# Optimization experiments

Measured on AMD Instinct MI355X. Metric: run time of the kernel, lower is better.

## Reference

```python
import jax, jax.numpy as jnp
import numpy as np

N_NODES = 100000


def gcn_conv(x, W, b, src, dst, n_nodes):
    # Linear transform first (PyG GCNConv applies weight before propagation)
    h = x @ W  # [N, out]
    # gcn_norm with self-loops: deg[i] = 1 + #incoming edges at i
    ones = jnp.ones(src.shape[0], dtype=h.dtype)
    deg = jax.ops.segment_sum(ones, dst, num_segments=n_nodes) + 1.0
    dinv = jax.lax.rsqrt(deg)  # deg^{-1/2}, deg >= 1 so safe
    norm = dinv[src] * dinv[dst]  # [E]
    # aggregate normalized messages at destination nodes
    agg = jax.ops.segment_sum(h[src] * norm[:, None], dst, num_segments=n_nodes)
    # self-loop contribution: norm_ii = dinv[i]^2
    agg = agg + h * (dinv * dinv)[:, None]
    return agg + b


def setup_inputs() -> dict:
    key = jax.random.key(0)
    k1, k2, k3, k4, k5, k6 = jax.random.split(key, 6)
    num_features, hidden, num_classes = 512, 128, 64
    x = jax.random.normal(k1, (N_NODES, num_features), dtype=jnp.float32)
    edge_index = jax.random.randint(k2, (2, 1600000), 0, N_NODES, dtype=jnp.int64)
    # Glorot-style params (scaled normals)
    W1 = jax.random.normal(k3, (num_features, hidden), dtype=jnp.float32) / np.sqrt(num_features)
    b1 = jnp.zeros((hidden,), dtype=jnp.float32)
    W2 = jax.random.normal(k4, (hidden, num_classes), dtype=jnp.float32) / np.sqrt(hidden)
    b2 = jnp.zeros((num_classes,), dtype=jnp.float32)
    return {"x": x, "edge_index": edge_index, "W1": W1, "b1": b1, "W2": W2, "b2": b2}


def reference(x, edge_index, W1, b1, W2, b2):
    src, dst = edge_index[0], edge_index[1]
    h = jax.nn.relu(gcn_conv(x, W1, b1, src, dst, N_NODES))
    out = gcn_conv(h, W2, b2, src, dst, N_NODES)
    return jax.nn.log_softmax(out, axis=1)
```

## Files before the change

### kernel.cpp

```cpp
#include <hip/hip_runtime.h>
#include <cmath>

#define N_NODES 100000
#define N_EDGES 1600000
#define F_IN 512
#define F_HID 128
#define F_OUT 64

#define BK_SHIFT 10
#define NBUK ((N_NODES + 1023) >> 10)
#define SCAP 24576
#define LSLOT 64
#define NBLK_A 512
#define FILL_SPLIT 8
#define NPS (1024 / FILL_SPLIT)
#define OV_CAP 4096

typedef __attribute__((ext_vector_type(8))) short short8;
typedef __attribute__((ext_vector_type(4))) float float4v;
typedef __attribute__((ext_vector_type(2))) float f2v;

#define GLOAD_LDS16(g, l)                                                      \
    __builtin_amdgcn_global_load_lds(                                          \
        (const __attribute__((address_space(1))) void*)(g),                    \
        (__attribute__((address_space(3))) void*)(l), 16, 0, 0)

__device__ __forceinline__ unsigned short f2bf(float f) {
    unsigned u = __builtin_bit_cast(unsigned, f);
    u += 0x7FFFu + ((u >> 16) & 1u);
    return (unsigned short)(u >> 16);
}
__device__ __forceinline__ float lo_bf(unsigned u) {
    return __builtin_bit_cast(float, u << 16);
}
__device__ __forceinline__ float hi_bf(unsigned u) {
    return __builtin_bit_cast(float, u & 0xFFFF0000u);
}
__device__ __forceinline__ f2v bfpair(unsigned u) {
    return f2v{__builtin_bit_cast(float, u << 16),
               __builtin_bit_cast(float, u & 0xFFFF0000u)};
}
__device__ __forceinline__ short8 cvt8(float4 lo, float4 hi) {
    return short8{(short)f2bf(lo.x), (short)f2bf(lo.y), (short)f2bf(lo.z), (short)f2bf(lo.w),
                  (short)f2bf(hi.x), (short)f2bf(hi.y), (short)f2bf(hi.z), (short)f2bf(hi.w)};
}
__device__ __forceinline__ unsigned pack_bf2(float a, float b) {
    return (unsigned)f2bf(a) | ((unsigned)f2bf(b) << 16);
}

template <int N>
__device__ __forceinline__ void waitvm() {
    if constexpr (N == 0) asm volatile("s_waitcnt vmcnt(0)" ::: "memory");
    else if constexpr (N == 3) asm volatile("s_waitcnt vmcnt(3)" ::: "memory");
    else if constexpr (N == 6) asm volatile("s_waitcnt vmcnt(6)" ::: "memory");
    else static_assert(N == 0 || N == 3 || N == 6, "add literal");
}
#define LGKM0() asm volatile("s_waitcnt lgkmcnt(0)" ::: "memory")
#define BAR() __builtin_amdgcn_s_barrier()
#define SCHED0() __builtin_amdgcn_sched_barrier(0)

__global__ __launch_bounds__(256) void partition_kernel(
    const int* __restrict__ src, const int* __restrict__ dst,
    unsigned* __restrict__ staging, int* __restrict__ gcur,
    unsigned long long* __restrict__ ovbuf, int* __restrict__ ovcnt) {
    __shared__ unsigned buf[NBUK][LSLOT];
    __shared__ int cnt[NBUK];
    int tid = threadIdx.x;
    for (int b = tid; b < NBUK; b += 256) cnt[b] = 0;
    __syncthreads();
    constexpr int PER = (((N_EDGES + NBLK_A - 1) / NBLK_A) + 3) & ~3;
    int e0 = blockIdx.x * PER;
    int e1 = min(e0 + PER, N_EDGES);

    auto body = [&](int d, int s) {
        int b = d >> BK_SHIFT;
        unsigned rec = (unsigned)s | ((unsigned)(d & 1023) << 17);
        int slot = atomicAdd(&cnt[b], 1);
        if (slot < LSLOT) {
            buf[b][slot] = rec;
        } else {
            int op = atomicAdd(ovcnt, 1);
            if (op < OV_CAP)
                ovbuf[op] = ((unsigned long long)(unsigned)d << 32) | (unsigned)s;
        }
    };
    auto drain = [&](void) {
        for (int b = tid; b < NBUK; b += 256) {
            int c = min(cnt[b], LSLOT);
            int full = c & ~15;
            if (full > 0) {
                int pos = atomicAdd(&gcur[b], full);
                if (pos + full <= SCAP) {
                    unsigned* dp = &staging[(size_t)b * SCAP + pos];
                    for (int i = 0; i < full; ++i) dp[i] = buf[b][i];
                }
                for (int i = 0; i < c - full; ++i) buf[b][i] = buf[b][full + i];
            }
            cnt[b] = c - full;
        }
    };

    int base = e0;
    for (; base + 1024 <= e1; base += 1024) {
        int e = base + tid * 4;
        int4 dv = *(const int4*)(dst + e);
        int4 sv = *(const int4*)(src + e);
        body(dv.x, sv.x);
        body(dv.y, sv.y);
        body(dv.z, sv.z);
        body(dv.w, sv.w);
        __syncthreads();
        drain();
        __syncthreads();
    }
    for (int e = base + tid; e < e1; e += 256) body(dst[e], src[e]);
    __syncthreads();
    drain();
    __syncthreads();
    for (int b = tid; b < NBUK; b += 256) {
        int c = cnt[b];
        if (c > 0) {
            int pos = atomicAdd(&gcur[b], c);
            if (pos + c <= SCAP)
                for (int i = 0; i < c; ++i) staging[(size_t)b * SCAP + pos + i] = buf[b][i];
        }
    }
}

__global__ __launch_bounds__(128) void bucket_scan_kernel(
    const int* __restrict__ gcur, const unsigned long long* __restrict__ ovbuf,
    const int* __restrict__ ovcnt, int* __restrict__ bucket_base,
    int* __restrict__ row_ptr) {
    __shared__ int ovc[128];
    __shared__ int sc[128];
    int tid = threadIdx.x;
    ovc[tid] = 0;
    int tot = (tid < NBUK) ? min(gcur[tid], SCAP) : 0;
    __syncthreads();
    int oc = *ovcnt;
    if (oc > OV_CAP) oc = OV_CAP;
    for (int k = tid; k < oc; k += 128)
        atomicAdd(&ovc[(int)(ovbuf[k] >> 32) >> BK_SHIFT], 1);
    __syncthreads();
    int v = tot + ovc[tid];
    sc[tid] = v;
    __syncthreads();
    for (int d = 1; d < 128; d <<= 1) {
        int u = (tid >= d) ? sc[tid - d] : 0;
        __syncthreads();
        sc[tid] += u;
        __syncthreads();
    }
    if (tid < NBUK) bucket_base[tid] = sc[tid] - v;
    if (tid == NBUK - 1) {
        bucket_base[NBUK] = sc[tid];
        row_ptr[N_NODES] = sc[tid];
    }
}

__global__ __launch_bounds__(256) void deg_hist_row_kernel(
    const unsigned* __restrict__ staging, const int* __restrict__ gcur,
    const unsigned long long* __restrict__ ovbuf, const int* __restrict__ ovcnt,
    const int* __restrict__ bucket_base, int* __restrict__ row_ptr,
    float* __restrict__ dinv) {
    int b = blockIdx.x;
    __shared__ int hist[1024];
    __shared__ int psum[256];
    int tid = threadIdx.x;
    for (int i = tid; i < 1024; i += 256) hist[i] = 0;
    __syncthreads();
    int n = gcur[b];
    if (n > SCAP) n = SCAP;
    const unsigned* sp = &staging[(size_t)b * SCAP];
    int i = tid * 4;
    for (; i + 4 <= n; i += 1024) {
        uint4 r = *(const uint4*)(sp + i);
        atomicAdd(&hist[r.x >> 17], 1);
        atomicAdd(&hist[r.y >> 17], 1);
        atomicAdd(&hist[r.z >> 17], 1);
        atomicAdd(&hist[r.w >> 17], 1);
    }
    int tail0 = n & ~3;
    if (tid < (n - tail0)) atomicAdd(&hist[sp[tail0 + tid] >> 17], 1);
    int oc = *ovcnt;
    if (oc > OV_CAP) oc = OV_CAP;
    for (int k = tid; k < oc; k += 256) {
        int d = (int)(ovbuf[k] >> 32);
        if ((d >> BK_SHIFT) == b) atomicAdd(&hist[d & 1023], 1);
    }
    __syncthreads();
    int i4 = tid * 4;
    int s0 = hist[i4], s1 = hist[i4 + 1], s2 = hist[i4 + 2], s3 = hist[i4 + 3];
    int ms = s0 + s1 + s2 + s3;
    psum[tid] = ms;
    __syncthreads();
    for (int d = 1; d < 256; d <<= 1) {
        int u = (tid >= d) ? psum[tid - d] : 0;
        __syncthreads();
        psum[tid] += u;
        __syncthreads();
    }
    int ex = psum[tid] - ms + bucket_base[b];
    int nd = (b << BK_SHIFT) + i4;
    if (nd < N_NODES) {
        row_ptr[nd]     = ex;
        row_ptr[nd + 1] = ex + s0;
        row_ptr[nd + 2] = ex + s0 + s1;
        row_ptr[nd + 3] = ex + s0 + s1 + s2;
        dinv[nd]     = rsqrtf((float)(s0 + 1));
        dinv[nd + 1] = rsqrtf((float)(s1 + 1));
        dinv[nd + 2] = rsqrtf((float)(s2 + 1));
        dinv[nd + 3] = rsqrtf((float)(s3 + 1));
    }
}

__global__ __launch_bounds__(256) void fill_kernel(
    const unsigned* __restrict__ staging, const int* __restrict__ gcur,
    const int* __restrict__ row_ptr, int* __restrict__ csr_src,
    const unsigned long long* __restrict__ ovbuf, const int* __restrict__ ovcnt) {
    int b = blockIdx.x / FILL_SPLIT;
    int slice = blockIdx.x - b * FILL_SPLIT;
    int dl0 = slice * NPS;
    int node0 = (b << BK_SHIFT) + dl0;
    __shared__ int lcur[NPS];
    int tid = threadIdx.x;
    if (tid < NPS) {
        int nd = node0 + tid;
        lcur[tid] = (nd < N_NODES) ? row_ptr[nd] : 0;
    }
    __syncthreads();

    int n = gcur[b];
    if (n > SCAP) n = SCAP;
    const unsigned* sp = &staging[(size_t)b * SCAP];

    auto process = [&](unsigned rec) {
        int dl = (int)(rec >> 17) - dl0;
        if ((unsigned)dl < (unsigned)NPS) {
            int pos = atomicAdd(&lcur[dl], 1);
            csr_src[pos] = (int)(rec & 0x1FFFFu);
        }
    };

    int i = tid * 4;
    for (; i + 4 <= n; i += 1024) {
        uint4 r = *(const uint4*)(sp + i);
        process(r.x);
        process(r.y);
        process(r.z);
        process(r.w);
    }
    int tail0 = n & ~3;
    if (tid < (n - tail0)) process(sp[tail0 + tid]);

    int oc = *ovcnt;
    if (oc > OV_CAP) oc = OV_CAP;
    for (int k = tid; k < oc; k += 256) {
        unsigned long long r = ovbuf[k];
        int d = (int)(r >> 32);
        int dl = d - node0;
        if ((d >> BK_SHIFT) == b && (unsigned)dl < (unsigned)NPS) {
            int pos = atomicAdd(&lcur[dl], 1);
            csr_src[pos] = (int)(r & 0xffffffffu);
        }
    }
}


__global__ void transpose_w_kernel(const float* __restrict__ W1, const float* __restrict__ W2,
                                   unsigned short* __restrict__ Wt1,
                                   unsigned short* __restrict__ Wt2) {
    int g = blockIdx.x * 256 + threadIdx.x;
    if (g < F_HID * F_IN) {
        int n = g >> 9, k = g & 511;
        Wt1[g] = f2bf(W1[k * F_HID + n]);
    } else {
        int h = g - F_HID * F_IN;
        if (h < F_OUT * F_HID) {
            int n = h >> 7, k = h & 127;
            Wt2[h] = f2bf(W2[k * F_OUT + n]);
        }
    }
}


template <int BN, int K, bool A_BF16>
__global__ __launch_bounds__(256, 3) void gemm_lds_kernel(
    const void* __restrict__ Araw, const unsigned short* __restrict__ Wt,
    const float* __restrict__ dinv, unsigned short* __restrict__ out, int N) {
    constexpr int NCT = BN / 16;
    constexpr int AE = A_BF16 ? 2 : 4;
    constexpr int SLOTS_A = (32 * AE) / 16;
    constexpr int MA = SLOTS_A - 1;
    constexpr int ABYTES = 128 * 32 * AE;
    constexpr int BBYTES = BN * 32 * 2;
    constexpr int NT = K / 32;
    constexpr int SL = (128 * SLOTS_A + BN * 4) / 256;

    __shared__ __align__(128) char Abuf[2][ABYTES];
    __shared__ __align__(128) char Bbuf[2][BBYTES];

    const char* Ab = (const char*)Araw;
    const char* Bb = (const char*)Wt;
    int tid = threadIdx.x;
    int lane = tid & 63;
    int wv = tid >> 6;
    int row0 = blockIdx.x * 128;
    int l15 = lane & 15;
    int q = lane >> 4;

    float4v acc[2][NCT] = {};

    auto stage = [&](int buf, int k0) {
        constexpr int CA = 128 * SLOTS_A;
#pragma unroll
        for (int i = 0; i < CA / 256; ++i) {
            int c = i * 256 + tid;
            int cw = i * 256 + (tid & ~63);
            int row = c / SLOTS_A;
            int s = c & MA;
            int g = s ^ (row & MA);
            int rg = row0 + row;
            if (rg >= N) rg = N - 1;
            GLOAD_LDS16(Ab + ((size_t)rg * K + k0) * AE + g * 16,
                        &Abuf[buf][cw * 16]);
        }
        constexpr int CB = BN * 4;
#pragma unroll
        for (int i = 0; i < CB / 256; ++i) {
            int c = i * 256 + tid;
            int cw = i * 256 + (tid & ~63);
            int col = c >> 2;
            int s = c & 3;
            int g = s ^ (col & 3);
            GLOAD_LDS16(Bb + ((size_t)col * K + k0) * 2 + g * 16,
                        &Bbuf[buf][cw * 16]);
        }
    };

    auto compute = [&](int buf) {
        const char* Ac = Abuf[buf];
        const char* Bc = Bbuf[buf];
        int lr0 = wv * 32 + l15;
        int lr1 = lr0 + 16;
        short8 a0, a1;
        if constexpr (A_BF16) {
            int s0 = q ^ (lr0 & 3);
            int s1 = q ^ (lr1 & 3);
            a0 = *(const short8*)(Ac + lr0 * 64 + s0 * 16);
            a1 = *(const short8*)(Ac + lr1 * 64 + s1 * 16);
        } else {
            int r7a = lr0 & 7, r7b = lr1 & 7;
            float4 f0 = *(const float4*)(Ac + lr0 * 128 + ((2 * q) ^ r7a) * 16);
            float4 f1 = *(const float4*)(Ac + lr0 * 128 + ((2 * q + 1) ^ r7a) * 16);
            float4 f2 = *(const float4*)(Ac + lr1 * 128 + ((2 * q) ^ r7b) * 16);
            float4 f3 = *(const float4*)(Ac + lr1 * 128 + ((2 * q + 1) ^ r7b) * 16);
            a0 = cvt8(f0, f1);
            a1 = cvt8(f2, f3);
        }
#pragma unroll
        for (int ct = 0; ct < NCT; ++ct) {
            int col = ct * 16 + l15;
            int sb = q ^ (col & 3);
            short8 b = *(const short8*)(Bc + col * 64 + sb * 16);
            acc[0][ct] = __builtin_amdgcn_mfma_f32_16x16x32_bf16(a0, b, acc[0][ct], 0, 0, 0);
            acc[1][ct] = __builtin_amdgcn_mfma_f32_16x16x32_bf16(a1, b, acc[1][ct], 0, 0, 0);
        }
    };

    stage(0, 0);
    stage(1, 32);
#pragma unroll 1
    for (int t = 0; t < NT - 2; ++t) {
        waitvm<SL>();
        BAR();
        SCHED0();
        compute(t & 1);
        LGKM0();
        BAR();
        SCHED0();
        stage(t & 1, (t + 2) * 32);
    }
    waitvm<SL>();
    BAR();
    SCHED0();
    compute((NT - 2) & 1);
    waitvm<0>();
    BAR();
    SCHED0();
    compute((NT - 1) & 1);

#pragma unroll
    for (int rt = 0; rt < 2; ++rt) {
#pragma unroll
        for (int reg = 0; reg < 4; ++reg) {
            int row = row0 + wv * 32 + rt * 16 + q * 4 + reg;
            if (row < N) {
                float sc = dinv[row];
#pragma unroll
                for (int ct = 0; ct < NCT; ++ct) {
                    out[(size_t)row * BN + ct * 16 + l15] = f2bf(acc[rt][ct][reg] * sc);
                }
            }
        }
    }
}


__global__ __launch_bounds__(256) void agg1_kernel(
    const uint4* __restrict__ g1v, const int* __restrict__ row_ptr,
    const int* __restrict__ csr_src, const float* __restrict__ dinv,
    const float4* __restrict__ b1v, uint4* __restrict__ h1v) {
    int tid = threadIdx.x;
    int wv = tid >> 6;
    int lane = tid & 63;
    int qt = lane >> 4;
    int ql = lane & 15;
    int node = blockIdx.x * 16 + wv * 4 + qt;
    uint4 u = g1v[(size_t)node * 16 + ql];
    f2v A0 = bfpair(u.x), A1 = bfpair(u.y), A2 = bfpair(u.z), A3 = bfpair(u.w);
    int e = row_ptr[node], end = row_ptr[node + 1];
#define GA1(j) g1v[(size_t)(j) * 16 + ql]
#define ACCV(v)                                                                \
    do { A0 += bfpair((v).x); A1 += bfpair((v).y);                             \
         A2 += bfpair((v).z); A3 += bfpair((v).w); } while (0)
    if (e + 8 <= end) {
        int j0 = csr_src[e], j1 = csr_src[e + 1], j2 = csr_src[e + 2], j3 = csr_src[e + 3];
        int j4 = csr_src[e + 4], j5 = csr_src[e + 5], j6 = csr_src[e + 6], j7 = csr_src[e + 7];
        uint4 v0 = GA1(j0), v1 = GA1(j1), v2 = GA1(j2), v3 = GA1(j3);
        uint4 v4 = GA1(j4), v5 = GA1(j5), v6 = GA1(j6), v7 = GA1(j7);
        e += 8;
        for (; e + 8 <= end; e += 8) {
            int k0 = csr_src[e], k1 = csr_src[e + 1], k2 = csr_src[e + 2], k3 = csr_src[e + 3];
            int k4 = csr_src[e + 4], k5 = csr_src[e + 5], k6 = csr_src[e + 6], k7 = csr_src[e + 7];
            ACCV(v0); ACCV(v1); ACCV(v2); ACCV(v3);
            ACCV(v4); ACCV(v5); ACCV(v6); ACCV(v7);
            v0 = GA1(k0); v1 = GA1(k1); v2 = GA1(k2); v3 = GA1(k3);
            v4 = GA1(k4); v5 = GA1(k5); v6 = GA1(k6); v7 = GA1(k7);
        }
        ACCV(v0); ACCV(v1); ACCV(v2); ACCV(v3);
        ACCV(v4); ACCV(v5); ACCV(v6); ACCV(v7);
    }
    for (; e < end; ++e) {
        uint4 v = GA1(csr_src[e]);
        ACCV(v);
    }
#undef ACCV
#undef GA1
    float d = dinv[node];
    float4 ba = b1v[2 * ql], bb = b1v[2 * ql + 1];
    float r0 = fmaxf(d * A0.x + ba.x, 0.0f), r1 = fmaxf(d * A0.y + ba.y, 0.0f);
    float r2 = fmaxf(d * A1.x + ba.z, 0.0f), r3 = fmaxf(d * A1.y + ba.w, 0.0f);
    float r4 = fmaxf(d * A2.x + bb.x, 0.0f), r5 = fmaxf(d * A2.y + bb.y, 0.0f);
    float r6 = fmaxf(d * A3.x + bb.z, 0.0f), r7 = fmaxf(d * A3.y + bb.w, 0.0f);
    h1v[(size_t)node * 16 + ql] =
        uint4{pack_bf2(r0, r1), pack_bf2(r2, r3), pack_bf2(r4, r5), pack_bf2(r6, r7)};
}

__global__ __launch_bounds__(256) void agg2_lsm_kernel(
    const uint2* __restrict__ g2v, const int* __restrict__ row_ptr,
    const int* __restrict__ csr_src, const float* __restrict__ dinv,
    const float4* __restrict__ b2v, float4* __restrict__ outv) {
    int tid = threadIdx.x;
    int wv = tid >> 6;
    int lane = tid & 63;
    int qt = lane >> 4;
    int ql = lane & 15;
    int node = blockIdx.x * 16 + wv * 4 + qt;
    uint2 u = g2v[(size_t)node * 16 + ql];
    f2v A0 = bfpair(u.x), A1 = bfpair(u.y);
    int e = row_ptr[node], end = row_ptr[node + 1];
#define GA2(j) g2v[(size_t)(j) * 16 + ql]
#define ACCV(v) do { A0 += bfpair((v).x); A1 += bfpair((v).y); } while (0)
    if (e + 8 <= end) {
        int j0 = csr_src[e], j1 = csr_src[e + 1], j2 = csr_src[e + 2], j3 = csr_src[e + 3];
        int j4 = csr_src[e + 4], j5 = csr_src[e + 5], j6 = csr_src[e + 6], j7 = csr_src[e + 7];
        uint2 v0 = GA2(j0), v1 = GA2(j1), v2 = GA2(j2), v3 = GA2(j3);
        uint2 v4 = GA2(j4), v5 = GA2(j5), v6 = GA2(j6), v7 = GA2(j7);
        e += 8;
        for (; e + 8 <= end; e += 8) {
            int k0 = csr_src[e], k1 = csr_src[e + 1], k2 = csr_src[e + 2], k3 = csr_src[e + 3];
            int k4 = csr_src[e + 4], k5 = csr_src[e + 5], k6 = csr_src[e + 6], k7 = csr_src[e + 7];
            ACCV(v0); ACCV(v1); ACCV(v2); ACCV(v3);
            ACCV(v4); ACCV(v5); ACCV(v6); ACCV(v7);
            v0 = GA2(k0); v1 = GA2(k1); v2 = GA2(k2); v3 = GA2(k3);
            v4 = GA2(k4); v5 = GA2(k5); v6 = GA2(k6); v7 = GA2(k7);
        }
        ACCV(v0); ACCV(v1); ACCV(v2); ACCV(v3);
        ACCV(v4); ACCV(v5); ACCV(v6); ACCV(v7);
    }
    for (; e < end; ++e) {
        uint2 v = GA2(csr_src[e]);
        ACCV(v);
    }
#undef ACCV
#undef GA2
    float d = dinv[node];
    float4 b = b2v[ql];
    float v0 = d * A0.x + b.x;
    float v1 = d * A0.y + b.y;
    float v2 = d * A1.x + b.z;
    float v3 = d * A1.y + b.w;
    float m = fmaxf(fmaxf(v0, v1), fmaxf(v2, v3));
#pragma unroll
    for (int o = 8; o > 0; o >>= 1) m = fmaxf(m, __shfl_xor(m, o, 64));
    float s = __expf(v0 - m) + __expf(v1 - m) + __expf(v2 - m) + __expf(v3 - m);
#pragma unroll
    for (int o = 8; o > 0; o >>= 1) s += __shfl_xor(s, o, 64);
    float ls = m + __logf(s);
    outv[(size_t)node * 16 + ql] = float4{v0 - ls, v1 - ls, v2 - ls, v3 - ls};
}


extern "C" void kernel_launch(void* const* d_in, const int* in_sizes, int n_in,
                              void* d_out, int out_size, void* d_ws, size_t ws_size,
                              hipStream_t stream) {
    const float* x  = (const float*)d_in[0];
    const int* eidx = (const int*)d_in[1];
    const float* W1 = (const float*)d_in[2];
    const float* b1 = (const float*)d_in[3];
    const float* W2 = (const float*)d_in[4];
    const float* b2 = (const float*)d_in[5];
    float* out = (float*)d_out;
    const int* src = eidx;
    const int* dst = eidx + N_EDGES;

    char* base = (char*)d_ws;
    size_t off = 0;
    auto alloc = [&](size_t bytes) -> void* {
        void* p = base + off;
        off += (bytes + 255) & ~(size_t)255;
        return p;
    };
    int* zbase    = (int*)alloc((size_t)(NBUK + 64) * 4);
    int* gcur     = zbase;
    int* ovcnt    = zbase + NBUK;
    int* bucket_base = (int*)alloc((size_t)(NBUK + 1) * 4);
    int* row_ptr  = (int*)alloc((size_t)(N_NODES + 1) * 4);
    float* dinv   = (float*)alloc((size_t)N_NODES * 4);
    unsigned* staging = (unsigned*)alloc((size_t)NBUK * SCAP * 4);
    unsigned long long* ovbuf = (unsigned long long*)alloc((size_t)OV_CAP * 8);
    int* csr_src  = (int*)alloc((size_t)N_EDGES * 4);
    unsigned short* Wt1 = (unsigned short*)alloc((size_t)F_HID * F_IN * 2);
    unsigned short* Wt2 = (unsigned short*)alloc((size_t)F_OUT * F_HID * 2);
    unsigned short* g1  = (unsigned short*)alloc((size_t)N_NODES * F_HID * 2);
    unsigned short* h1  = (unsigned short*)alloc((size_t)N_NODES * F_HID * 2);
    unsigned short* g2  = g1;

    hipMemsetAsync(zbase, 0, (size_t)(NBUK + 64) * 4, stream);
    partition_kernel<<<NBLK_A, 256, 0, stream>>>(src, dst, staging, gcur, ovbuf, ovcnt);
    bucket_scan_kernel<<<1, 128, 0, stream>>>(gcur, ovbuf, ovcnt, bucket_base, row_ptr);
    deg_hist_row_kernel<<<NBUK, 256, 0, stream>>>(staging, gcur, ovbuf, ovcnt,
                                                  bucket_base, row_ptr, dinv);
    fill_kernel<<<NBUK * FILL_SPLIT, 256, 0, stream>>>(staging, gcur, row_ptr, csr_src,
                                                       ovbuf, ovcnt);
    transpose_w_kernel<<<(F_HID * F_IN + F_OUT * F_HID + 255) / 256, 256, 0, stream>>>(
        W1, W2, Wt1, Wt2);

    int gblocks = (N_NODES + 127) / 128;
    gemm_lds_kernel<F_HID, F_IN, false><<<gblocks, 256, 0, stream>>>(
        (const void*)x, Wt1, dinv, g1, N_NODES);
    agg1_kernel<<<N_NODES / 16, 256, 0, stream>>>(
        (const uint4*)g1, row_ptr, csr_src, dinv, (const float4*)b1, (uint4*)h1);

    gemm_lds_kernel<F_OUT, F_HID, true><<<gblocks, 256, 0, stream>>>(
        (const void*)h1, Wt2, dinv, g2, N_NODES);
    agg2_lsm_kernel<<<N_NODES / 16, 256, 0, stream>>>(
        (const uint2*)g2, row_ptr, csr_src, dinv, (const float4*)b2, (float4*)out);
}
```

Baseline: 504.0 us.

## Replace incremental bucket drain with per-block fixed segments and count table

The partition kernel no longer drains its LDS buckets to global staging every 1024 edges with global atomics. Instead each block keeps up to 64 records per bucket in LDS and writes its whole buffer once to a private fixed segment, plus a per-bucket count table. The scan, histogram and fill kernels read the per-block segments using these counts. This removes repeated barriers, serial drain loops and global atomics, in exchange for sparse strided reads of a larger staging area and more reliance on the overflow buffer.

Measured after the change: 493.9 us. 2.0% less time.

```diff
diff --git a/kernel.cpp b/kernel.cpp
--- a/kernel.cpp
+++ b/kernel.cpp
@@ -9,9 +9,9 @@
 
 #define BK_SHIFT 10
 #define NBUK ((N_NODES + 1023) >> 10)
-#define SCAP 24576
-#define LSLOT 64
 #define NBLK_A 512
+#define PCAP 64
+#define SEGW (NBUK * PCAP)
 #define FILL_SPLIT 8
 #define NPS (1024 / FILL_SPLIT)
 #define OV_CAP 4096
@@ -61,9 +61,9 @@
 
 __global__ __launch_bounds__(256) void partition_kernel(
     const int* __restrict__ src, const int* __restrict__ dst,
-    unsigned* __restrict__ staging, int* __restrict__ gcur,
+    unsigned* __restrict__ staging, int* __restrict__ cnt_t,
     unsigned long long* __restrict__ ovbuf, int* __restrict__ ovcnt) {
-    __shared__ unsigned buf[NBUK][LSLOT];
+    __shared__ __align__(16) unsigned buf[NBUK][PCAP];
     __shared__ int cnt[NBUK];
     int tid = threadIdx.x;
     for (int b = tid; b < NBUK; b += 256) cnt[b] = 0;
@@ -76,27 +76,12 @@
         int b = d >> BK_SHIFT;
         unsigned rec = (unsigned)s | ((unsigned)(d & 1023) << 17);
         int slot = atomicAdd(&cnt[b], 1);
-        if (slot < LSLOT) {
+        if (slot < PCAP) {
             buf[b][slot] = rec;
         } else {
             int op = atomicAdd(ovcnt, 1);
             if (op < OV_CAP)
                 ovbuf[op] = ((unsigned long long)(unsigned)d << 32) | (unsigned)s;
-        }
-    };
-    auto drain = [&](void) {
-        for (int b = tid; b < NBUK; b += 256) {
-            int c = min(cnt[b], LSLOT);
-            int full = c & ~15;
-            if (full > 0) {
-                int pos = atomicAdd(&gcur[b], full);
-                if (pos + full <= SCAP) {
-                    unsigned* dp = &staging[(size_t)b * SCAP + pos];
-                    for (int i = 0; i < full; ++i) dp[i] = buf[b][i];
-                }
-                for (int i = 0; i < c - full; ++i) buf[b][i] = buf[b][full + i];
-            }
-            cnt[b] = c - full;
         }
     };
 
@@ -109,33 +94,32 @@
         body(dv.y, sv.y);
         body(dv.z, sv.z);
         body(dv.w, sv.w);
-        __syncthreads();
-        drain();
-        __syncthreads();
     }
     for (int e = base + tid; e < e1; e += 256) body(dst[e], src[e]);
     __syncthreads();
-    drain();
-    __syncthreads();
-    for (int b = tid; b < NBUK; b += 256) {
-        int c = cnt[b];
-        if (c > 0) {
-            int pos = atomicAdd(&gcur[b], c);
-            if (pos + c <= SCAP)
-                for (int i = 0; i < c; ++i) staging[(size_t)b * SCAP + pos + i] = buf[b][i];
-        }
-    }
+    const uint4* lb = (const uint4*)buf;
+    uint4* dp = (uint4*)(staging + (size_t)blockIdx.x * SEGW);
+    for (int i = tid; i < SEGW / 4; i += 256) dp[i] = lb[i];
+    for (int b = tid; b < NBUK; b += 256)
+        cnt_t[(size_t)b * NBLK_A + blockIdx.x] = min(cnt[b], PCAP);
 }
 
 __global__ __launch_bounds__(128) void bucket_scan_kernel(
-    const int* __restrict__ gcur, const unsigned long long* __restrict__ ovbuf,
+    const int* __restrict__ cnt_t, const unsigned long long* __restrict__ ovbuf,
     const int* __restrict__ ovcnt, int* __restrict__ bucket_base,
     int* __restrict__ row_ptr) {
     __shared__ int ovc[128];
     __shared__ int sc[128];
     int tid = threadIdx.x;
     ovc[tid] = 0;
-    int tot = (tid < NBUK) ? min(gcur[tid], SCAP) : 0;
+    int tot = 0;
+    if (tid < NBUK) {
+        const int4* p = (const int4*)(cnt_t + (size_t)tid * NBLK_A);
+        for (int i = 0; i < NBLK_A / 4; ++i) {
+            int4 v = p[i];
+            tot += v.x + v.y + v.z + v.w;
+        }
+    }
     __syncthreads();
     int oc = *ovcnt;
     if (oc > OV_CAP) oc = OV_CAP;
@@ -159,29 +143,31 @@
 }
 
 __global__ __launch_bounds__(256) void deg_hist_row_kernel(
-    const unsigned* __restrict__ staging, const int* __restrict__ gcur,
+    const unsigned* __restrict__ staging, const int* __restrict__ cnt_t,
     const unsigned long long* __restrict__ ovbuf, const int* __restrict__ ovcnt,
     const int* __restrict__ bucket_base, int* __restrict__ row_ptr,
     float* __restrict__ dinv) {
     int b = blockIdx.x;
     __shared__ int hist[1024];
     __shared__ int psum[256];
+    __shared__ unsigned char cntl[NBLK_A];
     int tid = threadIdx.x;
     for (int i = tid; i < 1024; i += 256) hist[i] = 0;
-    __syncthreads();
-    int n = gcur[b];
-    if (n > SCAP) n = SCAP;
-    const unsigned* sp = &staging[(size_t)b * SCAP];
-    int i = tid * 4;
-    for (; i + 4 <= n; i += 1024) {
-        uint4 r = *(const uint4*)(sp + i);
-        atomicAdd(&hist[r.x >> 17], 1);
-        atomicAdd(&hist[r.y >> 17], 1);
-        atomicAdd(&hist[r.z >> 17], 1);
-        atomicAdd(&hist[r.w >> 17], 1);
-    }
-    int tail0 = n & ~3;
-    if (tid < (n - tail0)) atomicAdd(&hist[sp[tail0 + tid] >> 17], 1);
+    for (int blk = tid; blk < NBLK_A; blk += 256)
+        cntl[blk] = (unsigned char)cnt_t[(size_t)b * NBLK_A + blk];
+    __syncthreads();
+    for (int qi = tid; qi < NBLK_A * (PCAP / 4); qi += 256) {
+        int blk = qi >> 4;
+        int s0 = (qi & 15) << 2;
+        int c = cntl[blk];
+        if (s0 < c) {
+            uint4 r = *(const uint4*)(staging + (size_t)blk * SEGW + b * PCAP + s0);
+            atomicAdd(&hist[r.x >> 17], 1);
+            if (s0 + 1 < c) atomicAdd(&hist[r.y >> 17], 1);
+            if (s0 + 2 < c) atomicAdd(&hist[r.z >> 17], 1);
+            if (s0 + 3 < c) atomicAdd(&hist[r.w >> 17], 1);
+        }
+    }
     int oc = *ovcnt;
     if (oc > OV_CAP) oc = OV_CAP;
     for (int k = tid; k < oc; k += 256) {
@@ -215,7 +201,7 @@
 }
 
 __global__ __launch_bounds__(256) void fill_kernel(
-    const unsigned* __restrict__ staging, const int* __restrict__ gcur,
+    const unsigned* __restrict__ staging, const int* __restrict__ cnt_t,
     const int* __restrict__ row_ptr, int* __restrict__ csr_src,
     const unsigned long long* __restrict__ ovbuf, const int* __restrict__ ovcnt) {
     int b = blockIdx.x / FILL_SPLIT;
@@ -223,16 +209,15 @@
     int dl0 = slice * NPS;
     int node0 = (b << BK_SHIFT) + dl0;
     __shared__ int lcur[NPS];
+    __shared__ unsigned char cntl[NBLK_A];
     int tid = threadIdx.x;
     if (tid < NPS) {
         int nd = node0 + tid;
         lcur[tid] = (nd < N_NODES) ? row_ptr[nd] : 0;
     }
-    __syncthreads();
-
-    int n = gcur[b];
-    if (n > SCAP) n = SCAP;
-    const unsigned* sp = &staging[(size_t)b * SCAP];
+    for (int blk = tid; blk < NBLK_A; blk += 256)
+        cntl[blk] = (unsigned char)cnt_t[(size_t)b * NBLK_A + blk];
+    __syncthreads();
 
     auto process = [&](unsigned rec) {
         int dl = (int)(rec >> 17) - dl0;
@@ -242,16 +227,18 @@
         }
     };
 
-    int i = tid * 4;
-    for (; i + 4 <= n; i += 1024) {
-        uint4 r = *(const uint4*)(sp + i);
-        process(r.x);
-        process(r.y);
-        process(r.z);
-        process(r.w);
-    }
-    int tail0 = n & ~3;
-    if (tid < (n - tail0)) process(sp[tail0 + tid]);
+    for (int qi = tid; qi < NBLK_A * (PCAP / 4); qi += 256) {
+        int blk = qi >> 4;
+        int s0 = (qi & 15) << 2;
+        int c = cntl[blk];
+        if (s0 < c) {
+            uint4 r = *(const uint4*)(staging + (size_t)blk * SEGW + b * PCAP + s0);
+            process(r.x);
+            if (s0 + 1 < c) process(r.y);
+            if (s0 + 2 < c) process(r.z);
+            if (s0 + 3 < c) process(r.w);
+        }
+    }
 
     int oc = *ovcnt;
     if (oc > OV_CAP) oc = OV_CAP;
@@ -532,13 +519,13 @@
         off += (bytes + 255) & ~(size_t)255;
         return p;
     };
-    int* zbase    = (int*)alloc((size_t)(NBUK + 64) * 4);
-    int* gcur     = zbase;
-    int* ovcnt    = zbase + NBUK;
+    int* zbase    = (int*)alloc((size_t)64 * 4);
+    int* ovcnt    = zbase;
+    int* cnt_t    = (int*)alloc((size_t)NBUK * NBLK_A * 4);
     int* bucket_base = (int*)alloc((size_t)(NBUK + 1) * 4);
     int* row_ptr  = (int*)alloc((size_t)(N_NODES + 1) * 4);
     float* dinv   = (float*)alloc((size_t)N_NODES * 4);
-    unsigned* staging = (unsigned*)alloc((size_t)NBUK * SCAP * 4);
+    unsigned* staging = (unsigned*)alloc((size_t)NBLK_A * SEGW * 4);
     unsigned long long* ovbuf = (unsigned long long*)alloc((size_t)OV_CAP * 8);
     int* csr_src  = (int*)alloc((size_t)N_EDGES * 4);
     unsigned short* Wt1 = (unsigned short*)alloc((size_t)F_HID * F_IN * 2);
@@ -547,12 +534,12 @@
     unsigned short* h1  = (unsigned short*)alloc((size_t)N_NODES * F_HID * 2);
     unsigned short* g2  = g1;
 
-    hipMemsetAsync(zbase, 0, (size_t)(NBUK + 64) * 4, stream);
-    partition_kernel<<<NBLK_A, 256, 0, stream>>>(src, dst, staging, gcur, ovbuf, ovcnt);
-    bucket_scan_kernel<<<1, 128, 0, stream>>>(gcur, ovbuf, ovcnt, bucket_base, row_ptr);
-    deg_hist_row_kernel<<<NBUK, 256, 0, stream>>>(staging, gcur, ovbuf, ovcnt,
+    hipMemsetAsync(zbase, 0, (size_t)64 * 4, stream);
+    partition_kernel<<<NBLK_A, 256, 0, stream>>>(src, dst, staging, cnt_t, ovbuf, ovcnt);
+    bucket_scan_kernel<<<1, 128, 0, stream>>>(cnt_t, ovbuf, ovcnt, bucket_base, row_ptr);
+    deg_hist_row_kernel<<<NBUK, 256, 0, stream>>>(staging, cnt_t, ovbuf, ovcnt,
                                                   bucket_base, row_ptr, dinv);
-    fill_kernel<<<NBUK * FILL_SPLIT, 256, 0, stream>>>(staging, gcur, row_ptr, csr_src,
+    fill_kernel<<<NBUK * FILL_SPLIT, 256, 0, stream>>>(staging, cnt_t, row_ptr, csr_src,
                                                        ovbuf, ovcnt);
     transpose_w_kernel<<<(F_HID * F_IN + F_OUT * F_HID + 255) / 256, 256, 0, stream>>>(
         W1, W2, Wt1, Wt2);
```
